# Kernel optimization log

Hardware: AMD Instinct MI355X
Metric: run time of the kernel (lower is better)

## Reference

```python
import jax, jax.numpy as jnp
import numpy as np

NUM_TOKENS = 16384
NUM_HEADS = 32
HEAD_SIZE = 128


def setup_inputs() -> dict:
    key = jax.random.key(0)
    k1, k2, k3, k4 = jax.random.split(key, 4)
    return {
        "prefix_output": jax.random.normal(k1, (NUM_TOKENS, NUM_HEADS, HEAD_SIZE), dtype=jnp.float32),
        "prefix_lse": jax.random.normal(k2, (NUM_HEADS, NUM_TOKENS), dtype=jnp.float32),
        "suffix_output": jax.random.normal(k3, (NUM_TOKENS, NUM_HEADS, HEAD_SIZE), dtype=jnp.float32),
        "suffix_lse": jax.random.normal(k4, (NUM_HEADS, NUM_TOKENS), dtype=jnp.float32),
    }


def reference(prefix_output, prefix_lse, suffix_output, suffix_lse):
    # transpose lse to [tokens, heads]
    p_lse = prefix_lse.T
    s_lse = suffix_lse.T
    neg_inf = jnp.array(-jnp.inf, dtype=p_lse.dtype)
    # +inf -> -inf sanitization (matches vLLM merge_attn_states)
    p_lse = jnp.where(jnp.isinf(p_lse) & (p_lse > 0), neg_inf, p_lse)
    s_lse = jnp.where(jnp.isinf(s_lse) & (s_lse > 0), neg_inf, s_lse)
    max_lse = jnp.maximum(p_lse, s_lse)
    p_se = jnp.exp(p_lse - max_lse)
    s_se = jnp.exp(s_lse - max_lse)
    out_se = p_se + s_se
    output_lse = (jnp.log(out_se) + max_lse).T  # [heads, tokens]
    p_scale = (p_se / out_se)[..., None]  # [tokens, heads, 1]
    s_scale = (s_se / out_se)[..., None]
    output = prefix_output * p_scale + suffix_output * s_scale
    return output, output_lse
```

## Files before the change

### kernel.cpp

```cpp
#include <hip/hip_runtime.h>
#include <math.h>

#define NUM_TOKENS 16384
#define NUM_HEADS  32
#define HEAD_SIZE  128

__global__ __launch_bounds__(256) void merge_attn_states_kernel(
    const float* __restrict__ p_out,
    const float* __restrict__ p_lse,
    const float* __restrict__ s_out,
    const float* __restrict__ s_lse,
    float* __restrict__ out,
    float* __restrict__ out_lse)
{
    const int pair = blockIdx.x * 8 + (threadIdx.x >> 5);
    const int lane = threadIdx.x & 31;
    const int head  = pair & (NUM_HEADS - 1);
    const int token = pair >> 5;

    const int lse_idx = head * NUM_TOKENS + token;

    float pl = p_lse[lse_idx];
    float sl = s_lse[lse_idx];
    if (isinf(pl) && pl > 0.0f) pl = -INFINITY;
    if (isinf(sl) && sl > 0.0f) sl = -INFINITY;

    const float m  = fmaxf(pl, sl);
    const float pe = expf(pl - m);
    const float se = expf(sl - m);
    const float denom = pe + se;
    const float inv_denom = 1.0f / denom;
    const float p_scale = pe * inv_denom;
    const float s_scale = se * inv_denom;

    if (lane == 0) {
        out_lse[lse_idx] = logf(denom) + m;
    }

    const size_t base = (size_t)pair * HEAD_SIZE;
    const float4* pv = reinterpret_cast<const float4*>(p_out + base);
    const float4* sv = reinterpret_cast<const float4*>(s_out + base);
    float4*       ov = reinterpret_cast<float4*>(out + base);

    float4 a = pv[lane];
    float4 b = sv[lane];
    float4 r;
    r.x = a.x * p_scale + b.x * s_scale;
    r.y = a.y * p_scale + b.y * s_scale;
    r.z = a.z * p_scale + b.z * s_scale;
    r.w = a.w * p_scale + b.w * s_scale;
    ov[lane] = r;
}

extern "C" void kernel_launch(void* const* d_in, const int* in_sizes, int n_in,
                              void* d_out, int out_size, void* d_ws, size_t ws_size,
                              hipStream_t stream) {
    const float* p_out = (const float*)d_in[0];
    const float* p_lse = (const float*)d_in[1];
    const float* s_out = (const float*)d_in[2];
    const float* s_lse = (const float*)d_in[3];

    float* out     = (float*)d_out;
    float* out_lse = (float*)d_out + (size_t)NUM_TOKENS * NUM_HEADS * HEAD_SIZE;

    const int total_pairs = NUM_TOKENS * NUM_HEADS;
    const int pairs_per_block = 256 / 32;
    const int blocks = total_pairs / pairs_per_block;

    merge_attn_states_kernel<<<blocks, 256, 0, stream>>>(
        p_out, p_lse, s_out, s_lse, out, out_lse);
}
```

Measured before the change: 140.3 us.

## Use grid-stride loop with 16 threads per head, two vec4 per thread

Replaces the one-block-per-8-pairs launch with a fixed 2048-block grid-stride loop. Each thread now handles two float4 chunks of a head vector, with 16 threads per (token, head) pair. The loads are issued before the LSE math, and fast intrinsics (__expf, rcp, __logf) replace the precise ones. The aim is to cut block scheduling overhead and get more bytes in flight per thread on a memory-bound kernel. The cost is slightly lower precision and the loop overhead.

```diff
diff --git a/kernel.cpp b/kernel.cpp
--- a/kernel.cpp
+++ b/kernel.cpp
@@ -4,8 +4,13 @@
 #define NUM_TOKENS 16384
 #define NUM_HEADS  32
 #define HEAD_SIZE  128
+#define TOTAL_PAIRS (NUM_TOKENS * NUM_HEADS)
+#define NBLOCKS  2048
+#define NTHREADS 256
 
-__global__ __launch_bounds__(256) void merge_attn_states_kernel(
+typedef float vfloat4 __attribute__((ext_vector_type(4)));
+
+__global__ __launch_bounds__(NTHREADS) void merge_attn_states_kernel(
     const float* __restrict__ p_out,
     const float* __restrict__ p_lse,
     const float* __restrict__ s_out,
@@ -13,43 +18,56 @@
     float* __restrict__ out,
     float* __restrict__ out_lse)
 {
-    const int pair = blockIdx.x * 8 + (threadIdx.x >> 5);
-    const int lane = threadIdx.x & 31;
-    const int head  = pair & (NUM_HEADS - 1);
-    const int token = pair >> 5;
+    const int stride = NBLOCKS * NTHREADS;
+    const int total  = TOTAL_PAIRS * 16;
 
-    const int lse_idx = head * NUM_TOKENS + token;
+    const vfloat4* __restrict__ pv = reinterpret_cast<const vfloat4*>(p_out);
+    const vfloat4* __restrict__ sv = reinterpret_cast<const vfloat4*>(s_out);
+    vfloat4* __restrict__ ov       = reinterpret_cast<vfloat4*>(out);
 
-    float pl = p_lse[lse_idx];
-    float sl = s_lse[lse_idx];
-    if (isinf(pl) && pl > 0.0f) pl = -INFINITY;
-    if (isinf(sl) && sl > 0.0f) sl = -INFINITY;
+    for (int idx = blockIdx.x * NTHREADS + threadIdx.x; idx < total; idx += stride) {
+        const int pair = idx >> 4;
+        const int sub  = idx & 15;
+        const int head  = pair & (NUM_HEADS - 1);
+        const int token = pair >> 5;
+        const int lse_idx = head * NUM_TOKENS + token;
 
-    const float m  = fmaxf(pl, sl);
-    const float pe = expf(pl - m);
-    const float se = expf(sl - m);
-    const float denom = pe + se;
-    const float inv_denom = 1.0f / denom;
-    const float p_scale = pe * inv_denom;
-    const float s_scale = se * inv_denom;
+        const int f0 = pair * 32 + sub;
+        const int f1 = f0 + 16;
+        vfloat4 a0 = pv[f0];
+        vfloat4 b0 = sv[f0];
+        vfloat4 a1 = pv[f1];
+        vfloat4 b1 = sv[f1];
 
-    if (lane == 0) {
-        out_lse[lse_idx] = logf(denom) + m;
+        float pl = p_lse[lse_idx];
+        float sl = s_lse[lse_idx];
+        if (isinf(pl) && pl > 0.0f) pl = -INFINITY;
+        if (isinf(sl) && sl > 0.0f) sl = -INFINITY;
+
+        const float m  = fmaxf(pl, sl);
+        const float pe = __expf(pl - m);
+        const float se = __expf(sl - m);
+        const float denom = pe + se;
+        const float inv   = __builtin_amdgcn_rcpf(denom);
+        const float ps = pe * inv;
+        const float ss = se * inv;
+
+        if (sub == 0) {
+            out_lse[lse_idx] = __logf(denom) + m;
+        }
+
+        vfloat4 r0, r1;
+        r0.x = fmaf(a0.x, ps, b0.x * ss);
+        r0.y = fmaf(a0.y, ps, b0.y * ss);
+        r0.z = fmaf(a0.z, ps, b0.z * ss);
+        r0.w = fmaf(a0.w, ps, b0.w * ss);
+        r1.x = fmaf(a1.x, ps, b1.x * ss);
+        r1.y = fmaf(a1.y, ps, b1.y * ss);
+        r1.z = fmaf(a1.z, ps, b1.z * ss);
+        r1.w = fmaf(a1.w, ps, b1.w * ss);
+        ov[f0] = r0;
+        ov[f1] = r1;
     }
-
-    const size_t base = (size_t)pair * HEAD_SIZE;
-    const float4* pv = reinterpret_cast<const float4*>(p_out + base);
-    const float4* sv = reinterpret_cast<const float4*>(s_out + base);
-    float4*       ov = reinterpret_cast<float4*>(out + base);
-
-    float4 a = pv[lane];
-    float4 b = sv[lane];
-    float4 r;
-    r.x = a.x * p_scale + b.x * s_scale;
-    r.y = a.y * p_scale + b.y * s_scale;
-    r.z = a.z * p_scale + b.z * s_scale;
-    r.w = a.w * p_scale + b.w * s_scale;
-    ov[lane] = r;
 }
 
 extern "C" void kernel_launch(void* const* d_in, const int* in_sizes, int n_in,
@@ -63,10 +81,6 @@
     float* out     = (float*)d_out;
     float* out_lse = (float*)d_out + (size_t)NUM_TOKENS * NUM_HEADS * HEAD_SIZE;
 
-    const int total_pairs = NUM_TOKENS * NUM_HEADS;
-    const int pairs_per_block = 256 / 32;
-    const int blocks = total_pairs / pairs_per_block;
-
-    merge_attn_states_kernel<<<blocks, 256, 0, stream>>>(
+    merge_attn_states_kernel<<<NBLOCKS, NTHREADS, 0, stream>>>(
         p_out, p_lse, s_out, s_lse, out, out_lse);
 }
```

New measurement: 161.6 us. +15.2%, slower.

## Split LSE merge into separate kernel writing per-pair scales to workspace

Applied to the files above, without the earlier changes.

Adds a first kernel that reads the head-major LSE arrays coalesced, computes the merged LSE and the two per-pair scale factors, and stores the scales token-major in the workspace. A second kernel then does the flat vectorized output merge, reading one float2 scale per pair. The aim is to replace the strided transposed LSE reads of the original kernel with coalesced ones. In exchange it adds a second launch and a small workspace round trip. Fast-math exp, log and reciprocal intrinsics are also used, and a fallback single kernel runs if the workspace is too small.

```diff
diff --git a/kernel.cpp b/kernel.cpp
--- a/kernel.cpp
+++ b/kernel.cpp
@@ -4,51 +4,97 @@
 #define NUM_TOKENS 16384
 #define NUM_HEADS  32
 #define HEAD_SIZE  128
+#define TOTAL_PAIRS (NUM_TOKENS * NUM_HEADS)
+#define TOTAL_F4    (TOTAL_PAIRS * (HEAD_SIZE / 4))
+#define NTHREADS 256
 
-__global__ __launch_bounds__(256) void merge_attn_states_kernel(
+typedef float vfloat2 __attribute__((ext_vector_type(2)));
+typedef float vfloat4 __attribute__((ext_vector_type(4)));
+
+__global__ __launch_bounds__(NTHREADS) void lse_merge_kernel(
+    const float* __restrict__ p_lse,
+    const float* __restrict__ s_lse,
+    float* __restrict__ out_lse,
+    vfloat2* __restrict__ scales)
+{
+    const int tid = blockIdx.x * NTHREADS + threadIdx.x;
+    const int head  = tid >> 14;
+    const int token = tid & (NUM_TOKENS - 1);
+    const int pair  = token * NUM_HEADS + head;
+
+    float pl = p_lse[tid];
+    float sl = s_lse[tid];
+    if (isinf(pl) && pl > 0.0f) pl = -INFINITY;
+    if (isinf(sl) && sl > 0.0f) sl = -INFINITY;
+
+    const float m  = fmaxf(pl, sl);
+    const float pe = __expf(pl - m);
+    const float se = __expf(sl - m);
+    const float d  = pe + se;
+    const float inv = __builtin_amdgcn_rcpf(d);
+
+    out_lse[tid] = __logf(d) + m;
+    vfloat2 sc;
+    sc.x = pe * inv;
+    sc.y = se * inv;
+    scales[pair] = sc;
+}
+
+__global__ __launch_bounds__(NTHREADS) void merge_out_kernel(
     const float* __restrict__ p_out,
-    const float* __restrict__ p_lse,
     const float* __restrict__ s_out,
-    const float* __restrict__ s_lse,
-    float* __restrict__ out,
-    float* __restrict__ out_lse)
+    const vfloat2* __restrict__ scales,
+    float* __restrict__ out)
+{
+    const int idx  = blockIdx.x * NTHREADS + threadIdx.x;
+    const int pair = idx >> 5;
+
+    const vfloat4* __restrict__ pv = reinterpret_cast<const vfloat4*>(p_out);
+    const vfloat4* __restrict__ sv = reinterpret_cast<const vfloat4*>(s_out);
+    vfloat4* __restrict__ ov       = reinterpret_cast<vfloat4*>(out);
+
+    vfloat2 sc = scales[pair];
+    vfloat4 a  = pv[idx];
+    vfloat4 b  = sv[idx];
+
+    vfloat4 r;
+    r.x = fmaf(a.x, sc.x, b.x * sc.y);
+    r.y = fmaf(a.y, sc.x, b.y * sc.y);
+    r.z = fmaf(a.z, sc.x, b.z * sc.y);
+    r.w = fmaf(a.w, sc.x, b.w * sc.y);
+    ov[idx] = r;
+}
+
+__global__ __launch_bounds__(NTHREADS) void merge_fallback_kernel(
+    const float* __restrict__ p_out, const float* __restrict__ p_lse,
+    const float* __restrict__ s_out, const float* __restrict__ s_lse,
+    float* __restrict__ out, float* __restrict__ out_lse)
 {
     const int pair = blockIdx.x * 8 + (threadIdx.x >> 5);
     const int lane = threadIdx.x & 31;
-    const int head  = pair & (NUM_HEADS - 1);
-    const int token = pair >> 5;
-
-    const int lse_idx = head * NUM_TOKENS + token;
+    const int lse_idx = (pair & (NUM_HEADS - 1)) * NUM_TOKENS + (pair >> 5);
 
     float pl = p_lse[lse_idx];
     float sl = s_lse[lse_idx];
     if (isinf(pl) && pl > 0.0f) pl = -INFINITY;
     if (isinf(sl) && sl > 0.0f) sl = -INFINITY;
-
     const float m  = fmaxf(pl, sl);
-    const float pe = expf(pl - m);
-    const float se = expf(sl - m);
-    const float denom = pe + se;
-    const float inv_denom = 1.0f / denom;
-    const float p_scale = pe * inv_denom;
-    const float s_scale = se * inv_denom;
-
-    if (lane == 0) {
-        out_lse[lse_idx] = logf(denom) + m;
-    }
+    const float pe = __expf(pl - m);
+    const float se = __expf(sl - m);
+    const float d  = pe + se;
+    const float inv = __builtin_amdgcn_rcpf(d);
+    const float ps = pe * inv, ss = se * inv;
+    if (lane == 0) out_lse[lse_idx] = __logf(d) + m;
 
     const size_t base = (size_t)pair * HEAD_SIZE;
-    const float4* pv = reinterpret_cast<const float4*>(p_out + base);
-    const float4* sv = reinterpret_cast<const float4*>(s_out + base);
-    float4*       ov = reinterpret_cast<float4*>(out + base);
-
-    float4 a = pv[lane];
-    float4 b = sv[lane];
-    float4 r;
-    r.x = a.x * p_scale + b.x * s_scale;
-    r.y = a.y * p_scale + b.y * s_scale;
-    r.z = a.z * p_scale + b.z * s_scale;
-    r.w = a.w * p_scale + b.w * s_scale;
+    const vfloat4* pv = reinterpret_cast<const vfloat4*>(p_out + base);
+    const vfloat4* sv = reinterpret_cast<const vfloat4*>(s_out + base);
+    vfloat4*       ov = reinterpret_cast<vfloat4*>(out + base);
+    vfloat4 a = pv[lane], b = sv[lane], r;
+    r.x = fmaf(a.x, ps, b.x * ss);
+    r.y = fmaf(a.y, ps, b.y * ss);
+    r.z = fmaf(a.z, ps, b.z * ss);
+    r.w = fmaf(a.w, ps, b.w * ss);
     ov[lane] = r;
 }
 
@@ -63,10 +109,16 @@
     float* out     = (float*)d_out;
     float* out_lse = (float*)d_out + (size_t)NUM_TOKENS * NUM_HEADS * HEAD_SIZE;
 
-    const int total_pairs = NUM_TOKENS * NUM_HEADS;
-    const int pairs_per_block = 256 / 32;
-    const int blocks = total_pairs / pairs_per_block;
+    const size_t scales_bytes = (size_t)TOTAL_PAIRS * sizeof(vfloat2);
 
-    merge_attn_states_kernel<<<blocks, 256, 0, stream>>>(
-        p_out, p_lse, s_out, s_lse, out, out_lse);
+    if (ws_size >= scales_bytes) {
+        vfloat2* scales = (vfloat2*)d_ws;
+        lse_merge_kernel<<<TOTAL_PAIRS / NTHREADS, NTHREADS, 0, stream>>>(
+            p_lse, s_lse, out_lse, scales);
+        merge_out_kernel<<<TOTAL_F4 / NTHREADS, NTHREADS, 0, stream>>>(
+            p_out, s_out, scales, out);
+    } else {
+        merge_fallback_kernel<<<TOTAL_PAIRS / 8, NTHREADS, 0, stream>>>(
+            p_out, p_lse, s_out, s_lse, out, out_lse);
+    }
 }
```

After: 145.1 us. 1.03x slower.

## Remap work head-major, issue loads early, use fast math and nontemporal stores

Applied to the files above, without the earlier changes.

Work items are now ordered head-major, so each block's 8 groups read consecutive tokens for one head. LSE reads and writes become coalesced, while the big tensor reads now stride across tokens at 16KB intervals. The vector loads are issued before the LSE math, the math uses fast intrinsics (__expf, rcp, __logf), and the output store is nontemporal to avoid polluting the cache. The new ordering risks poorer DRAM page locality on the main output tensors, and the fast intrinsics give slightly less exact results.

```diff
diff --git a/kernel.cpp b/kernel.cpp
--- a/kernel.cpp
+++ b/kernel.cpp
@@ -4,8 +4,12 @@
 #define NUM_TOKENS 16384
 #define NUM_HEADS  32
 #define HEAD_SIZE  128
+#define TOTAL_PAIRS (NUM_TOKENS * NUM_HEADS)
+#define NTHREADS 256
 
-__global__ __launch_bounds__(256) void merge_attn_states_kernel(
+typedef float vfloat4 __attribute__((ext_vector_type(4)));
+
+__global__ __launch_bounds__(NTHREADS) void merge_attn_states_kernel(
     const float* __restrict__ p_out,
     const float* __restrict__ p_lse,
     const float* __restrict__ s_out,
@@ -13,43 +17,41 @@
     float* __restrict__ out,
     float* __restrict__ out_lse)
 {
-    const int pair = blockIdx.x * 8 + (threadIdx.x >> 5);
+    const int gid  = blockIdx.x * 8 + (threadIdx.x >> 5);
     const int lane = threadIdx.x & 31;
-    const int head  = pair & (NUM_HEADS - 1);
-    const int token = pair >> 5;
+    const int head  = gid >> 14;
+    const int token = gid & (NUM_TOKENS - 1);
+    const int pair  = token * NUM_HEADS + head;
 
-    const int lse_idx = head * NUM_TOKENS + token;
+    const size_t base = (size_t)pair * HEAD_SIZE;
+    const vfloat4* __restrict__ pv = reinterpret_cast<const vfloat4*>(p_out + base);
+    const vfloat4* __restrict__ sv = reinterpret_cast<const vfloat4*>(s_out + base);
+    vfloat4 a = pv[lane];
+    vfloat4 b = sv[lane];
+    float pl = p_lse[gid];
+    float sl = s_lse[gid];
 
-    float pl = p_lse[lse_idx];
-    float sl = s_lse[lse_idx];
-    if (isinf(pl) && pl > 0.0f) pl = -INFINITY;
-    if (isinf(sl) && sl > 0.0f) sl = -INFINITY;
+    pl = (pl == INFINITY) ? -INFINITY : pl;
+    sl = (sl == INFINITY) ? -INFINITY : sl;
 
     const float m  = fmaxf(pl, sl);
-    const float pe = expf(pl - m);
-    const float se = expf(sl - m);
-    const float denom = pe + se;
-    const float inv_denom = 1.0f / denom;
-    const float p_scale = pe * inv_denom;
-    const float s_scale = se * inv_denom;
+    const float pe = __expf(pl - m);
+    const float se = __expf(sl - m);
+    const float d  = pe + se;
+    const float inv = __builtin_amdgcn_rcpf(d);
+    const float ps = pe * inv;
+    const float ss = se * inv;
 
     if (lane == 0) {
-        out_lse[lse_idx] = logf(denom) + m;
+        out_lse[gid] = __logf(d) + m;
     }
 
-    const size_t base = (size_t)pair * HEAD_SIZE;
-    const float4* pv = reinterpret_cast<const float4*>(p_out + base);
-    const float4* sv = reinterpret_cast<const float4*>(s_out + base);
-    float4*       ov = reinterpret_cast<float4*>(out + base);
-
-    float4 a = pv[lane];
-    float4 b = sv[lane];
-    float4 r;
-    r.x = a.x * p_scale + b.x * s_scale;
-    r.y = a.y * p_scale + b.y * s_scale;
-    r.z = a.z * p_scale + b.z * s_scale;
-    r.w = a.w * p_scale + b.w * s_scale;
-    ov[lane] = r;
+    vfloat4 r;
+    r.x = fmaf(a.x, ps, b.x * ss);
+    r.y = fmaf(a.y, ps, b.y * ss);
+    r.z = fmaf(a.z, ps, b.z * ss);
+    r.w = fmaf(a.w, ps, b.w * ss);
+    __builtin_nontemporal_store(r, reinterpret_cast<vfloat4*>(out + base) + lane);
 }
 
 extern "C" void kernel_launch(void* const* d_in, const int* in_sizes, int n_in,
@@ -63,10 +65,7 @@
     float* out     = (float*)d_out;
     float* out_lse = (float*)d_out + (size_t)NUM_TOKENS * NUM_HEADS * HEAD_SIZE;
 
-    const int total_pairs = NUM_TOKENS * NUM_HEADS;
-    const int pairs_per_block = 256 / 32;
-    const int blocks = total_pairs / pairs_per_block;
-
-    merge_attn_states_kernel<<<blocks, 256, 0, stream>>>(
+    const int blocks = TOTAL_PAIRS / 8;
+    merge_attn_states_kernel<<<blocks, NTHREADS, 0, stream>>>(
         p_out, p_lse, s_out, s_lse, out, out_lse);
 }
```

Result: slower. 148.5 us (+5.8%).
